# Optimization experiments

Hardware: AMD Instinct MI355X
Metric: run time of the kernel (lower is better)

## Reference

```python
import jax, jax.numpy as jnp
import numpy as np

B, L, D = 2, 2048, 1024
H, G = 16, 2            # num_heads, num_kv_groups
HPG = H // G            # heads per kv group = 8
DQK, DV = 128, 128      # qk_head_dim, v_head_dim (head_dim=64, ratios=2.0)


def setup_inputs() -> dict:
    key = jax.random.key(0)
    ks = jax.random.split(key, 12)

    def xavier(k, shape, scale=1.0):
        fan_in, fan_out = shape[0], shape[1]
        lim = np.sqrt(6.0 / (fan_in + fan_out))
        return jax.random.uniform(k, shape, jnp.float32, -lim, lim) * scale

    return {
        "in_q": jax.random.normal(ks[0], (B, L, D), jnp.float32),
        "in_k": jax.random.normal(ks[1], (B, L, D), jnp.float32),
        "in_v": jax.random.normal(ks[2], (B, L, D), jnp.float32),
        # weights stored as [in, out] (transpose of torch Linear); qk_init_scale=0.5
        "Wq": xavier(ks[3], (D, H * DQK), 0.5),
        "bq": jnp.zeros((H * DQK,), jnp.float32),
        "Wk": xavier(ks[4], (D, G * DQK), 0.5),
        "bk": jnp.zeros((G * DQK,), jnp.float32),
        "Wv": xavier(ks[5], (D, G * DV)),
        "bv": jnp.zeros((G * DV,), jnp.float32),
        "Wo": xavier(ks[6], (H * DV, D)),
        "bo": jnp.zeros((D,), jnp.float32),
        "q_extra_scale": jnp.ones((1,), jnp.float32),
    }


def reference(in_q, in_k, in_v, Wq, bq, Wk, bk, Wv, bv, Wo, bo, q_extra_scale):
    # fused projections
    q = (in_q @ Wq + bq) * q_extra_scale              # [B,L,H*DQK]
    k = in_k @ Wk + bk                                 # [B,L,G*DQK]
    v = in_v @ Wv + bv                                 # [B,L,G*DV]

    # reshape: keep GQA group structure instead of materializing repeat_interleave
    q = q.reshape(B, L, G, HPG, DQK)                   # heads grouped: head h = g*HPG + m
    k = k.reshape(B, L, G, DQK)
    v = v.reshape(B, L, G, DV)

    scale = 1.0 / np.sqrt(DQK)
    # scores: [B,G,HPG,L_q,L_kv]
    scores = jnp.einsum("bsgmd,btgd->bgmst", q, k) * scale
    causal = jnp.tril(jnp.ones((L, L), bool))          # is_causal=True
    scores = jnp.where(causal, scores, jnp.finfo(scores.dtype).min)
    attn = jax.nn.softmax(scores, axis=-1)
    ctx = jnp.einsum("bgmst,btgd->bsgmd", attn, v)     # [B,L,G,HPG,DV]
    ctx = ctx.reshape(B, L, H * DV)
    return ctx @ Wo + bo                               # [B,L,D]
```

## Files before the change

### kernel.cpp

```cpp
#include <hip/hip_runtime.h>


typedef __bf16 bf16;
typedef __bf16 bf16x8 __attribute__((ext_vector_type(8)));
typedef __bf16 bf16x4 __attribute__((ext_vector_type(4)));
typedef float f32x4 __attribute__((ext_vector_type(4)));
typedef float f32x16 __attribute__((ext_vector_type(16)));
typedef float float4v __attribute__((ext_vector_type(4)));

#define MFMA_BF16(a, b, c) __builtin_amdgcn_mfma_f32_16x16x32_bf16((a), (b), (c), 0, 0, 0)
#define MFMA32(a, b, c)    __builtin_amdgcn_mfma_f32_32x32x16_bf16((a), (b), (c), 0, 0, 0)

static constexpr int Bz = 2, Lz = 2048, Dz = 1024;
static constexpr int Hz = 16, Gz = 2;
static constexpr int DQKz = 128, DVz = 128;

__device__ __forceinline__ void async_copy16(const bf16* g, bf16* l) {
    __builtin_amdgcn_global_load_lds(
        (const __attribute__((address_space(1))) unsigned int*)g,
        (__attribute__((address_space(3))) unsigned int*)l, 16, 0, 0);
}

__device__ __forceinline__ unsigned cvt_pk_bf16(float lo, float hi) {
    unsigned r;
    asm("v_cvt_pk_bf16_f32 %0, %1, %2" : "=v"(r) : "v"(lo), "v"(hi));
    return r;
}

__global__ __launch_bounds__(256) void prep(
    const float* __restrict__ q, const float* __restrict__ k,
    const float* __restrict__ v, bf16* __restrict__ dq,
    bf16* __restrict__ dk, bf16* __restrict__ dv,
    const float* __restrict__ Wq, const float* __restrict__ Wk,
    const float* __restrict__ Wv, const float* __restrict__ Wo,
    bf16* __restrict__ WqT, bf16* __restrict__ WkT,
    bf16* __restrict__ WvT, bf16* __restrict__ WoT)
{
    int bid = blockIdx.x;
    if (bid < 6144) {
        const float* s = bid < 2048 ? q : (bid < 4096 ? k : v);
        bf16* d = bid < 2048 ? dq : (bid < 4096 ? dk : dv);
        int i = (bid & 2047) * 2048 + threadIdx.x * 8;
        float4v a = *(const float4v*)(s + i);
        float4v b = *(const float4v*)(s + i + 4);
        bf16x8 o;
        #pragma unroll
        for (int j = 0; j < 4; ++j) { o[j] = (bf16)a[j]; o[j + 4] = (bf16)b[j]; }
        *(bf16x8*)(d + i) = o;
        return;
    }
    bid -= 6144;
    const float* W; bf16* WT; int K, N;
    if (bid < 2048)      { W = Wq; WT = WqT; K = 1024; N = 2048; }
    else if (bid < 2304) { W = Wk; WT = WkT; K = 1024; N = 256;  bid -= 2048; }
    else if (bid < 2560) { W = Wv; WT = WvT; K = 1024; N = 256;  bid -= 2304; }
    else                 { W = Wo; WT = WoT; K = 2048; N = 1024; bid -= 2560; }
    int tiles_n = N >> 5;
    int n0 = (bid % tiles_n) * 32, k0 = (bid / tiles_n) * 32;

    __shared__ bf16 t[32][33];
    int tx = threadIdx.x & 31, ty = threadIdx.x >> 5;
    #pragma unroll
    for (int i = 0; i < 4; ++i)
        t[ty + i * 8][tx] = (bf16)W[(size_t)(k0 + ty + i * 8) * N + n0 + tx];
    __syncthreads();
    #pragma unroll
    for (int i = 0; i < 4; ++i)
        WT[(size_t)(n0 + ty + i * 8) * K + k0 + tx] = t[tx][ty + i * 8];
}

template <typename TC>
__device__ __forceinline__ void gemm_tile(
    const bf16* __restrict__ A, const bf16* __restrict__ BT,
    const float* __restrict__ bias, float scale, TC* __restrict__ C,
    int M, int N, int K, int m0, int n0, bool trans_out,
    bf16 (&As)[2][128 * 64], bf16 (&Bs)[2][128 * 64])
{
    const int tid  = threadIdx.x;
    const int wave = tid >> 6;
    const int lane = tid & 63;
    const int quad = lane >> 4;
    const int l16  = lane & 15;
    const int sw   = l16 & 7;
    const int wm = wave >> 2, wn = wave & 3;

    f32x4 acc[4][2] = {};

    auto stage = [&](int k0, int buf) {
        #pragma unroll
        for (int s = 0; s < 2; ++s) {
            int i = s * 512 + tid;
            int row = i >> 3, c = (i & 7) ^ (row & 7);
            async_copy16(A + (size_t)(m0 + row) * K + k0 + c * 8, &As[buf][i * 8]);
        }
        #pragma unroll
        for (int s = 0; s < 2; ++s) {
            int i = s * 512 + tid;
            int row = i >> 3, c = (i & 7) ^ (row & 7);
            async_copy16(BT + (size_t)(n0 + row) * K + k0 + c * 8, &Bs[buf][i * 8]);
        }
    };

    stage(0, 0);
    int cur = 0;
    for (int k0 = 0; k0 < K; k0 += 64) {
        __syncthreads();
        if (k0 + 64 < K) stage(k0 + 64, cur ^ 1);

        #pragma unroll
        for (int ks = 0; ks < 2; ++ks) {
            bf16x8 af[4], bfv[2];
            #pragma unroll
            for (int mt = 0; mt < 4; ++mt)
                af[mt] = *(const bf16x8*)(&As[cur][((wm * 64 + mt * 16 + l16) * 8
                                                    + ((ks * 4 + quad) ^ sw)) * 8]);
            #pragma unroll
            for (int nt = 0; nt < 2; ++nt)
                bfv[nt] = *(const bf16x8*)(&Bs[cur][((wn * 32 + nt * 16 + l16) * 8
                                                     + ((ks * 4 + quad) ^ sw)) * 8]);
            #pragma unroll
            for (int mt = 0; mt < 4; ++mt)
                #pragma unroll
                for (int nt = 0; nt < 2; ++nt)
                    acc[mt][nt] = MFMA_BF16(af[mt], bfv[nt], acc[mt][nt]);
        }
        cur ^= 1;
    }

    #pragma unroll
    for (int nt = 0; nt < 2; ++nt) {
        int col = n0 + wn * 32 + nt * 16 + l16;
        float bv = bias[col];
        #pragma unroll
        for (int mt = 0; mt < 4; ++mt) {
            int row = m0 + wm * 64 + mt * 16 + quad * 4;
            if (trans_out) {
                struct V4 { TC v[4]; } o;
                #pragma unroll
                for (int r = 0; r < 4; ++r)
                    o.v[r] = (TC)((acc[mt][nt][r] + bv) * scale);
                *(V4*)(&C[(size_t)col * M + row]) = o;
            } else {
                #pragma unroll
                for (int r = 0; r < 4; ++r)
                    C[(size_t)(row + r) * N + col] =
                        (TC)((acc[mt][nt][r] + bv) * scale);
            }
        }
    }
}

__global__ __launch_bounds__(512, 4) void proj_qkv(
    const bf16* __restrict__ aq, const bf16* __restrict__ ak,
    const bf16* __restrict__ av, const bf16* __restrict__ WqT,
    const bf16* __restrict__ WkT, const bf16* __restrict__ WvT,
    const float* __restrict__ bq, const float* __restrict__ bk,
    const float* __restrict__ bv, const float* __restrict__ qsc,
    bf16* __restrict__ Qw, bf16* __restrict__ Kw, bf16* __restrict__ VwT)
{
    __shared__ bf16 As[2][128 * 64];
    __shared__ bf16 Bs[2][128 * 64];
    int bid = blockIdx.x;
    if (bid < 512) {
        float scale = qsc[0] * 0.08838834764831845f * 1.4426950408889634f;
        gemm_tile<bf16>(aq, WqT, bq, scale, Qw, 4096, 2048, 1024,
                        (bid >> 4) * 128, (bid & 15) * 128, false, As, Bs);
    } else if (bid < 576) {
        int b2 = bid - 512;
        gemm_tile<bf16>(ak, WkT, bk, 1.0f, Kw, 4096, 256, 1024,
                        (b2 >> 1) * 128, (b2 & 1) * 128, false, As, Bs);
    } else {
        int b2 = bid - 576;
        gemm_tile<bf16>(av, WvT, bv, 1.0f, VwT, 4096, 256, 1024,
                        (b2 >> 1) * 128, (b2 & 1) * 128, true, As, Bs);
    }
}

__global__ __launch_bounds__(512, 4) void proj_o(
    const bf16* __restrict__ Cw, const bf16* __restrict__ WoT,
    const float* __restrict__ bo, float* __restrict__ out)
{
    __shared__ bf16 As[2][128 * 64];
    __shared__ bf16 Bs[2][128 * 64];
    gemm_tile<float>(Cw, WoT, bo, 1.0f, out, 4096, 1024, 2048,
                     (blockIdx.x >> 3) * 128, (blockIdx.x & 7) * 128,
                     false, As, Bs);
}

__global__ __launch_bounds__(256, 3) void attn_fused(
    const bf16* __restrict__ Q,
    const bf16* __restrict__ Kp,
    const bf16* __restrict__ VT,
    bf16* __restrict__ ctx)
{
    __shared__ bf16 smem[24576];

    const int tid  = threadIdx.x;
    const int wave = tid >> 6;
    const int lane = tid & 63;
    const int hi   = lane >> 5;
    const int l31  = lane & 31;
    const int s7   = l31 & 7;
    const int wq   = wave >> 1;
    const int kvw  = wave & 1;

    const int h = blockIdx.y;
    const int b = blockIdx.z;
    const int g = h >> 3;

    const bf16* kgbase = Kp + (size_t)(b * Lz) * (Gz * DQKz) + g * DQKz;
    const bf16* vgbase = VT + (size_t)(g * DVz) * (Bz * Lz) + b * Lz;

    int kgo[4], vgo[4], ldso[4];
    #pragma unroll
    for (int s = 0; s < 4; ++s) {
        int i = s * 256 + tid;
        ldso[s] = i * 8;
        int key = i >> 4, ck = (i & 15) ^ (key & 7);
        kgo[s] = key * (Gz * DQKz) + ck * 8;
        int dvr = i >> 3, cv = (i & 7) ^ (dvr & 7);
        vgo[s] = dvr * (Bz * Lz) + cv * 8;
    }
    auto stage_K = [&](int kt) {
        const bf16* kb = kgbase + (size_t)(kt * 64) * (Gz * DQKz);
        #pragma unroll
        for (int s = 0; s < 4; ++s) async_copy16(kb + kgo[s], smem + ldso[s]);
    };
    auto stage_V = [&](int kt, int buf) {
        const bf16* vb = vgbase + kt * 64;
        #pragma unroll
        for (int s = 0; s < 4; ++s)
            async_copy16(vb + vgo[s], smem + 8192 + buf * 8192 + ldso[s]);
    };

    int koff[8];
    #pragma unroll
    for (int ks = 0; ks < 8; ++ks)
        koff[ks] = ((kvw * 32 + l31) * 16 + ((ks * 2 + hi) ^ s7)) * 8;
    int voff[4][2];
    #pragma unroll
    for (int dt = 0; dt < 4; ++dt)
        #pragma unroll
        for (int kss = 0; kss < 2; ++kss)
            voff[dt][kss] = ((dt * 32 + l31) * 8
                             + ((kvw * 4 + kss * 2 + hi) ^ s7)) * 8;

    const int qt  = 31 - (int)blockIdx.x;
    const int q0  = qt * 64;
    const int nkt = qt + 1;
    const int qrow = q0 + wq * 32 + l31;

    bf16x8 qf[8];
    {
        const bf16* qbase = Q + (size_t)(b * Lz + qrow) * (Hz * DQKz) + h * DQKz;
        #pragma unroll
        for (int s = 0; s < 8; ++s)
            qf[s] = *(const bf16x8*)(qbase + s * 16 + hi * 8);
    }

    f32x16 oacc0 = {}, oacc1 = {}, oacc2 = {}, oacc3 = {};
    float lsum = 0.0f;

    stage_K(0);
    stage_V(0, 0);
    int cur = 0;

    for (int kt = 0; kt < nkt; ++kt) {
        __syncthreads();

        const bf16* vcur = smem + 8192 + cur * 8192;

        f32x16 sacc = {};
        __builtin_amdgcn_s_setprio(1);
        #pragma unroll
        for (int ks = 0; ks < 8; ++ks) {
            bf16x8 kf = *(const bf16x8*)(smem + koff[ks]);
            sacc = MFMA32(kf, qf[ks], sacc);
        }
        __builtin_amdgcn_s_setprio(0);

        __syncthreads();
        if (kt + 1 < nkt) {
            stage_K(kt + 1);
            stage_V(kt + 1, cur ^ 1);
        }

        float pv[16];
        if (kt == nkt - 1) {
            #pragma unroll
            for (int r = 0; r < 16; ++r) {
                int key = kvw * 32 + (r & 3) + 8 * (r >> 2) + 4 * hi;
                pv[r] = (key > wq * 32 + l31) ? 0.0f
                                              : exp2f(sacc[r] - 8.0f);
            }
        } else {
            #pragma unroll
            for (int r = 0; r < 16; ++r)
                pv[r] = exp2f(sacc[r] - 8.0f);
        }
        lsum += ((pv[0] + pv[1]) + (pv[2] + pv[3]))
              + ((pv[4] + pv[5]) + (pv[6] + pv[7]))
              + ((pv[8] + pv[9]) + (pv[10] + pv[11]))
              + ((pv[12] + pv[13]) + (pv[14] + pv[15]));

        unsigned c0 = cvt_pk_bf16(pv[0],  pv[1]);
        unsigned c1 = cvt_pk_bf16(pv[2],  pv[3]);
        unsigned c2 = cvt_pk_bf16(pv[4],  pv[5]);
        unsigned c3 = cvt_pk_bf16(pv[6],  pv[7]);
        unsigned c4 = cvt_pk_bf16(pv[8],  pv[9]);
        unsigned c5 = cvt_pk_bf16(pv[10], pv[11]);
        unsigned c6 = cvt_pk_bf16(pv[12], pv[13]);
        unsigned c7 = cvt_pk_bf16(pv[14], pv[15]);
        asm("v_permlane32_swap_b32 %0, %1" : "+v"(c0), "+v"(c2));
        asm("v_permlane32_swap_b32 %0, %1" : "+v"(c1), "+v"(c3));
        asm("v_permlane32_swap_b32 %0, %1" : "+v"(c4), "+v"(c6));
        asm("v_permlane32_swap_b32 %0, %1" : "+v"(c5), "+v"(c7));
        union { unsigned u[4]; bf16x8 v; } p0 = {{c0, c1, c2, c3}};
        union { unsigned u[4]; bf16x8 v; } p1 = {{c4, c5, c6, c7}};

        __builtin_amdgcn_s_setprio(1);
        {
            bf16x8 vf;
            vf = *(const bf16x8*)(vcur + voff[0][0]); oacc0 = MFMA32(vf, p0.v, oacc0);
            vf = *(const bf16x8*)(vcur + voff[0][1]); oacc0 = MFMA32(vf, p1.v, oacc0);
            vf = *(const bf16x8*)(vcur + voff[1][0]); oacc1 = MFMA32(vf, p0.v, oacc1);
            vf = *(const bf16x8*)(vcur + voff[1][1]); oacc1 = MFMA32(vf, p1.v, oacc1);
            vf = *(const bf16x8*)(vcur + voff[2][0]); oacc2 = MFMA32(vf, p0.v, oacc2);
            vf = *(const bf16x8*)(vcur + voff[2][1]); oacc2 = MFMA32(vf, p1.v, oacc2);
            vf = *(const bf16x8*)(vcur + voff[3][0]); oacc3 = MFMA32(vf, p0.v, oacc3);
            vf = *(const bf16x8*)(vcur + voff[3][1]); oacc3 = MFMA32(vf, p1.v, oacc3);
        }
        __builtin_amdgcn_s_setprio(0);
        cur ^= 1;
    }

    lsum += __shfl_xor(lsum, 32);

    float* SM = (float*)smem;
    float* E0 = SM;
    float* E1 = SM + 5120;
    float* LS = SM + 10240;
    __syncthreads();

    auto store_partial = [&](f32x16 v, float* E) {
        #pragma unroll
        for (int j = 0; j < 4; ++j) {
            f32x4 v4 = { v[4 * j], v[4 * j + 1], v[4 * j + 2], v[4 * j + 3] };
            *(f32x4*)&E[(wave * 64 + lane) * 20 + 4 * j] = v4;
        }
    };
    if (kvw == 0) { store_partial(oacc2, E0); store_partial(oacc3, E1); }
    else          { store_partial(oacc0, E0); store_partial(oacc1, E1); }
    if (lane < 32) LS[wave * 32 + lane] = lsum;
    __syncthreads();
    lsum += LS[(wave ^ 1) * 32 + l31];
    const float inv = 1.0f / lsum;

    bf16* cbase = ctx + (size_t)(b * Lz + qrow) * (Hz * DVz) + h * DVz;
    auto finalize = [&](f32x16 v, float* E, int dt) {
        #pragma unroll
        for (int j = 0; j < 4; ++j) {
            f32x4 p4 = *(const f32x4*)&E[((wave ^ 1) * 64 + lane) * 20 + 4 * j];
            bf16x4 o4;
            #pragma unroll
            for (int r = 0; r < 4; ++r)
                o4[r] = (bf16)((v[4 * j + r] + p4[r]) * inv);
            *(bf16x4*)&cbase[dt * 32 + j * 8 + hi * 4] = o4;
        }
    };
    if (kvw == 0) { finalize(oacc0, E0, 0); finalize(oacc1, E1, 1); }
    else          { finalize(oacc2, E0, 2); finalize(oacc3, E1, 3); }
}

extern "C" void kernel_launch(void* const* d_in, const int* in_sizes, int n_in,
                              void* d_out, int out_size, void* d_ws, size_t ws_size,
                              hipStream_t stream)
{
    (void)in_sizes; (void)n_in; (void)out_size; (void)ws_size;

    const float* in_q = (const float*)d_in[0];
    const float* in_k = (const float*)d_in[1];
    const float* in_v = (const float*)d_in[2];
    const float* Wq   = (const float*)d_in[3];
    const float* bq   = (const float*)d_in[4];
    const float* Wk   = (const float*)d_in[5];
    const float* bk   = (const float*)d_in[6];
    const float* Wv   = (const float*)d_in[7];
    const float* bv   = (const float*)d_in[8];
    const float* Wo   = (const float*)d_in[9];
    const float* bo   = (const float*)d_in[10];
    const float* qsc  = (const float*)d_in[11];
    float* out = (float*)d_out;

    const int M = Bz * Lz;
    const int NQ = Hz * DQKz;
    const int NKV = Gz * DQKz;

    bf16* aq  = (bf16*)d_ws;
    bf16* WqT = aq  + (size_t)M * Dz;
    bf16* WkT = WqT + (size_t)NQ * Dz;
    bf16* WvT = WkT + (size_t)NKV * Dz;
    bf16* WoT = WvT + (size_t)NKV * Dz;
    bf16* Qw  = WoT + (size_t)Dz * NQ;
    bf16* Kw  = Qw  + (size_t)M * NQ;
    bf16* VwT = Kw  + (size_t)M * NKV;
    bf16* Cw  = VwT + (size_t)NKV * M;
    bf16* ak  = Cw;
    bf16* av  = Cw + (size_t)M * Dz;

    prep<<<dim3(10752), dim3(256), 0, stream>>>(
        in_q, in_k, in_v, aq, ak, av, Wq, Wk, Wv, Wo, WqT, WkT, WvT, WoT);

    proj_qkv<<<dim3(640), dim3(512), 0, stream>>>(
        aq, ak, av, WqT, WkT, WvT, bq, bk, bv, qsc, Qw, Kw, VwT);

    attn_fused<<<dim3(32, Hz, Bz), dim3(256), 0, stream>>>(Qw, Kw, VwT, Cw);

    proj_o<<<dim3(256), dim3(512), 0, stream>>>(Cw, WoT, bo, out);
}
```

Baseline: 281.7 us.

## Pair causal query tiles per block and software-pipeline QK with double-buffered K

```diff
diff --git a/kernel.cpp b/kernel.cpp
--- a/kernel.cpp
+++ b/kernel.cpp
@@ -187,13 +187,13 @@
                      false, As, Bs);
 }
 
-__global__ __launch_bounds__(256, 3) void attn_fused(
+__global__ __launch_bounds__(256, 2) void attn_fused(
     const bf16* __restrict__ Q,
     const bf16* __restrict__ Kp,
     const bf16* __restrict__ VT,
     bf16* __restrict__ ctx)
 {
-    __shared__ bf16 smem[24576];
+    __shared__ bf16 smem[32768];
 
     const int tid  = threadIdx.x;
     const int wave = tid >> 6;
@@ -221,16 +221,17 @@
         int dvr = i >> 3, cv = (i & 7) ^ (dvr & 7);
         vgo[s] = dvr * (Bz * Lz) + cv * 8;
     }
-    auto stage_K = [&](int kt) {
+    auto stage_K = [&](int kt, int buf) {
         const bf16* kb = kgbase + (size_t)(kt * 64) * (Gz * DQKz);
         #pragma unroll
-        for (int s = 0; s < 4; ++s) async_copy16(kb + kgo[s], smem + ldso[s]);
+        for (int s = 0; s < 4; ++s)
+            async_copy16(kb + kgo[s], smem + buf * 8192 + ldso[s]);
     };
     auto stage_V = [&](int kt, int buf) {
         const bf16* vb = vgbase + kt * 64;
         #pragma unroll
         for (int s = 0; s < 4; ++s)
-            async_copy16(vb + vgo[s], smem + 8192 + buf * 8192 + ldso[s]);
+            async_copy16(vb + vgo[s], smem + 16384 + buf * 8192 + ldso[s]);
     };
 
     int koff[8];
@@ -245,131 +246,149 @@
             voff[dt][kss] = ((dt * 32 + l31) * 8
                              + ((kvw * 4 + kss * 2 + hi) ^ s7)) * 8;
 
-    const int qt  = 31 - (int)blockIdx.x;
-    const int q0  = qt * 64;
-    const int nkt = qt + 1;
-    const int qrow = q0 + wq * 32 + l31;
-
-    bf16x8 qf[8];
-    {
-        const bf16* qbase = Q + (size_t)(b * Lz + qrow) * (Hz * DQKz) + h * DQKz;
-        #pragma unroll
-        for (int s = 0; s < 8; ++s)
-            qf[s] = *(const bf16x8*)(qbase + s * 16 + hi * 8);
-    }
-
-    f32x16 oacc0 = {}, oacc1 = {}, oacc2 = {}, oacc3 = {};
-    float lsum = 0.0f;
-
-    stage_K(0);
-    stage_V(0, 0);
-    int cur = 0;
-
-    for (int kt = 0; kt < nkt; ++kt) {
+    for (int pass = 0; pass < 2; ++pass) {
+        const int qt  = pass == 0 ? (31 - (int)blockIdx.x) : (int)blockIdx.x;
+        const int q0  = qt * 64;
+        const int nkt = qt + 1;
+        const int qrow = q0 + wq * 32 + l31;
+
+        bf16x8 qf[8];
+        {
+            const bf16* qbase = Q + (size_t)(b * Lz + qrow) * (Hz * DQKz) + h * DQKz;
+            #pragma unroll
+            for (int s = 0; s < 8; ++s)
+                qf[s] = *(const bf16x8*)(qbase + s * 16 + hi * 8);
+        }
+
+        f32x16 oacc0 = {}, oacc1 = {}, oacc2 = {}, oacc3 = {};
+        f32x16 saccA = {}, saccB = {};
+        float lsum = 0.0f;
+
+        if (pass) __syncthreads();
+        stage_K(0, 0);
+        stage_V(0, 0);
+        if (nkt > 1) stage_K(1, 1);
         __syncthreads();
 
-        const bf16* vcur = smem + 8192 + cur * 8192;
-
-        f32x16 sacc = {};
-        __builtin_amdgcn_s_setprio(1);
-        #pragma unroll
-        for (int ks = 0; ks < 8; ++ks) {
-            bf16x8 kf = *(const bf16x8*)(smem + koff[ks]);
-            sacc = MFMA32(kf, qf[ks], sacc);
-        }
-        __builtin_amdgcn_s_setprio(0);
-
+        {
+            f32x16 s = {};
+            #pragma unroll
+            for (int ks = 0; ks < 8; ++ks) {
+                bf16x8 kf = *(const bf16x8*)(smem + koff[ks]);
+                s = MFMA32(kf, qf[ks], s);
+            }
+            saccA = s;
+        }
+
+        auto iter_body = [&](int t, f32x16& scur, f32x16& snxt) {
+            __syncthreads();
+            if (t + 2 < nkt) stage_K(t + 2, t & 1);
+            if (t + 1 < nkt) stage_V(t + 1, (t + 1) & 1);
+
+            if (t + 1 < nkt) {
+                const bf16* kc = smem + ((t + 1) & 1) * 8192;
+                f32x16 s = {};
+                #pragma unroll
+                for (int ks = 0; ks < 8; ++ks) {
+                    bf16x8 kf = *(const bf16x8*)(kc + koff[ks]);
+                    s = MFMA32(kf, qf[ks], s);
+                }
+                snxt = s;
+            }
+
+            float pv[16];
+            if (t == nkt - 1) {
+                #pragma unroll
+                for (int r = 0; r < 16; ++r) {
+                    int key = kvw * 32 + (r & 3) + 8 * (r >> 2) + 4 * hi;
+                    pv[r] = (key > wq * 32 + l31) ? 0.0f
+                                                  : exp2f(scur[r] - 8.0f);
+                }
+            } else {
+                #pragma unroll
+                for (int r = 0; r < 16; ++r)
+                    pv[r] = exp2f(scur[r] - 8.0f);
+            }
+            lsum += ((pv[0] + pv[1]) + (pv[2] + pv[3]))
+                  + ((pv[4] + pv[5]) + (pv[6] + pv[7]))
+                  + ((pv[8] + pv[9]) + (pv[10] + pv[11]))
+                  + ((pv[12] + pv[13]) + (pv[14] + pv[15]));
+
+            unsigned c0 = cvt_pk_bf16(pv[0],  pv[1]);
+            unsigned c1 = cvt_pk_bf16(pv[2],  pv[3]);
+            unsigned c2 = cvt_pk_bf16(pv[4],  pv[5]);
+            unsigned c3 = cvt_pk_bf16(pv[6],  pv[7]);
+            unsigned c4 = cvt_pk_bf16(pv[8],  pv[9]);
+            unsigned c5 = cvt_pk_bf16(pv[10], pv[11]);
+            unsigned c6 = cvt_pk_bf16(pv[12], pv[13]);
+            unsigned c7 = cvt_pk_bf16(pv[14], pv[15]);
+            asm("v_permlane32_swap_b32 %0, %1" : "+v"(c0), "+v"(c2));
+            asm("v_permlane32_swap_b32 %0, %1" : "+v"(c1), "+v"(c3));
+            asm("v_permlane32_swap_b32 %0, %1" : "+v"(c4), "+v"(c6));
+            asm("v_permlane32_swap_b32 %0, %1" : "+v"(c5), "+v"(c7));
+            union { unsigned u[4]; bf16x8 v; } p0 = {{c0, c1, c2, c3}};
+            union { unsigned u[4]; bf16x8 v; } p1 = {{c4, c5, c6, c7}};
+
+            const bf16* vcur = smem + 16384 + (t & 1) * 8192;
+            __builtin_amdgcn_s_setprio(1);
+            {
+                bf16x8 vf;
+                vf = *(const bf16x8*)(vcur + voff[0][0]); oacc0 = MFMA32(vf, p0.v, oacc0);
+                vf = *(const bf16x8*)(vcur + voff[0][1]); oacc0 = MFMA32(vf, p1.v, oacc0);
+                vf = *(const bf16x8*)(vcur + voff[1][0]); oacc1 = MFMA32(vf, p0.v, oacc1);
+                vf = *(const bf16x8*)(vcur + voff[1][1]); oacc1 = MFMA32(vf, p1.v, oacc1);
+                vf = *(const bf16x8*)(vcur + voff[2][0]); oacc2 = MFMA32(vf, p0.v, oacc2);
+                vf = *(const bf16x8*)(vcur + voff[2][1]); oacc2 = MFMA32(vf, p1.v, oacc2);
+                vf = *(const bf16x8*)(vcur + voff[3][0]); oacc3 = MFMA32(vf, p0.v, oacc3);
+                vf = *(const bf16x8*)(vcur + voff[3][1]); oacc3 = MFMA32(vf, p1.v, oacc3);
+            }
+            __builtin_amdgcn_s_setprio(0);
+        };
+
+        int t = 0;
+        for (; t + 2 <= nkt; t += 2) {
+            iter_body(t,     saccA, saccB);
+            iter_body(t + 1, saccB, saccA);
+        }
+        if (nkt & 1) iter_body(nkt - 1, saccA, saccB);
+
+        lsum += __shfl_xor(lsum, 32);
+
+        float* SM = (float*)smem;
+        float* E0 = SM;
+        float* E1 = SM + 5120;
+        float* LS = SM + 10240;
         __syncthreads();
-        if (kt + 1 < nkt) {
-            stage_K(kt + 1);
-            stage_V(kt + 1, cur ^ 1);
-        }
-
-        float pv[16];
-        if (kt == nkt - 1) {
-            #pragma unroll
-            for (int r = 0; r < 16; ++r) {
-                int key = kvw * 32 + (r & 3) + 8 * (r >> 2) + 4 * hi;
-                pv[r] = (key > wq * 32 + l31) ? 0.0f
-                                              : exp2f(sacc[r] - 8.0f);
-            }
-        } else {
-            #pragma unroll
-            for (int r = 0; r < 16; ++r)
-                pv[r] = exp2f(sacc[r] - 8.0f);
-        }
-        lsum += ((pv[0] + pv[1]) + (pv[2] + pv[3]))
-              + ((pv[4] + pv[5]) + (pv[6] + pv[7]))
-              + ((pv[8] + pv[9]) + (pv[10] + pv[11]))
-              + ((pv[12] + pv[13]) + (pv[14] + pv[15]));
-
-        unsigned c0 = cvt_pk_bf16(pv[0],  pv[1]);
-        unsigned c1 = cvt_pk_bf16(pv[2],  pv[3]);
-        unsigned c2 = cvt_pk_bf16(pv[4],  pv[5]);
-        unsigned c3 = cvt_pk_bf16(pv[6],  pv[7]);
-        unsigned c4 = cvt_pk_bf16(pv[8],  pv[9]);
-        unsigned c5 = cvt_pk_bf16(pv[10], pv[11]);
-        unsigned c6 = cvt_pk_bf16(pv[12], pv[13]);
-        unsigned c7 = cvt_pk_bf16(pv[14], pv[15]);
-        asm("v_permlane32_swap_b32 %0, %1" : "+v"(c0), "+v"(c2));
-        asm("v_permlane32_swap_b32 %0, %1" : "+v"(c1), "+v"(c3));
-        asm("v_permlane32_swap_b32 %0, %1" : "+v"(c4), "+v"(c6));
-        asm("v_permlane32_swap_b32 %0, %1" : "+v"(c5), "+v"(c7));
-        union { unsigned u[4]; bf16x8 v; } p0 = {{c0, c1, c2, c3}};
-        union { unsigned u[4]; bf16x8 v; } p1 = {{c4, c5, c6, c7}};
-
-        __builtin_amdgcn_s_setprio(1);
-        {
-            bf16x8 vf;
-            vf = *(const bf16x8*)(vcur + voff[0][0]); oacc0 = MFMA32(vf, p0.v, oacc0);
-            vf = *(const bf16x8*)(vcur + voff[0][1]); oacc0 = MFMA32(vf, p1.v, oacc0);
-            vf = *(const bf16x8*)(vcur + voff[1][0]); oacc1 = MFMA32(vf, p0.v, oacc1);
-            vf = *(const bf16x8*)(vcur + voff[1][1]); oacc1 = MFMA32(vf, p1.v, oacc1);
-            vf = *(const bf16x8*)(vcur + voff[2][0]); oacc2 = MFMA32(vf, p0.v, oacc2);
-            vf = *(const bf16x8*)(vcur + voff[2][1]); oacc2 = MFMA32(vf, p1.v, oacc2);
-            vf = *(const bf16x8*)(vcur + voff[3][0]); oacc3 = MFMA32(vf, p0.v, oacc3);
-            vf = *(const bf16x8*)(vcur + voff[3][1]); oacc3 = MFMA32(vf, p1.v, oacc3);
-        }
-        __builtin_amdgcn_s_setprio(0);
-        cur ^= 1;
-    }
-
-    lsum += __shfl_xor(lsum, 32);
-
-    float* SM = (float*)smem;
-    float* E0 = SM;
-    float* E1 = SM + 5120;
-    float* LS = SM + 10240;
-    __syncthreads();
-
-    auto store_partial = [&](f32x16 v, float* E) {
-        #pragma unroll
-        for (int j = 0; j < 4; ++j) {
-            f32x4 v4 = { v[4 * j], v[4 * j + 1], v[4 * j + 2], v[4 * j + 3] };
-            *(f32x4*)&E[(wave * 64 + lane) * 20 + 4 * j] = v4;
-        }
-    };
-    if (kvw == 0) { store_partial(oacc2, E0); store_partial(oacc3, E1); }
-    else          { store_partial(oacc0, E0); store_partial(oacc1, E1); }
-    if (lane < 32) LS[wave * 32 + lane] = lsum;
-    __syncthreads();
-    lsum += LS[(wave ^ 1) * 32 + l31];
-    const float inv = 1.0f / lsum;
-
-    bf16* cbase = ctx + (size_t)(b * Lz + qrow) * (Hz * DVz) + h * DVz;
-    auto finalize = [&](f32x16 v, float* E, int dt) {
-        #pragma unroll
-        for (int j = 0; j < 4; ++j) {
-            f32x4 p4 = *(const f32x4*)&E[((wave ^ 1) * 64 + lane) * 20 + 4 * j];
-            bf16x4 o4;
-            #pragma unroll
-            for (int r = 0; r < 4; ++r)
-                o4[r] = (bf16)((v[4 * j + r] + p4[r]) * inv);
-            *(bf16x4*)&cbase[dt * 32 + j * 8 + hi * 4] = o4;
-        }
-    };
-    if (kvw == 0) { finalize(oacc0, E0, 0); finalize(oacc1, E1, 1); }
-    else          { finalize(oacc2, E0, 2); finalize(oacc3, E1, 3); }
+
+        auto store_partial = [&](f32x16 v, float* E) {
+            #pragma unroll
+            for (int j = 0; j < 4; ++j) {
+                f32x4 v4 = { v[4 * j], v[4 * j + 1], v[4 * j + 2], v[4 * j + 3] };
+                *(f32x4*)&E[(wave * 64 + lane) * 20 + 4 * j] = v4;
+            }
+        };
+        if (kvw == 0) { store_partial(oacc2, E0); store_partial(oacc3, E1); }
+        else          { store_partial(oacc0, E0); store_partial(oacc1, E1); }
+        if (lane < 32) LS[wave * 32 + lane] = lsum;
+        __syncthreads();
+        lsum += LS[(wave ^ 1) * 32 + l31];
+        const float inv = 1.0f / lsum;
+
+        bf16* cbase = ctx + (size_t)(b * Lz + qrow) * (Hz * DVz) + h * DVz;
+        auto finalize = [&](f32x16 v, float* E, int dt) {
+            #pragma unroll
+            for (int j = 0; j < 4; ++j) {
+                f32x4 p4 = *(const f32x4*)&E[((wave ^ 1) * 64 + lane) * 20 + 4 * j];
+                bf16x4 o4;
+                #pragma unroll
+                for (int r = 0; r < 4; ++r)
+                    o4[r] = (bf16)((v[4 * j + r] + p4[r]) * inv);
+                *(bf16x4*)&cbase[dt * 32 + j * 8 + hi * 4] = o4;
+            }
+        };
+        if (kvw == 0) { finalize(oacc0, E0, 0); finalize(oacc1, E1, 1); }
+        else          { finalize(oacc2, E0, 2); finalize(oacc3, E1, 3); }
+    }
 }
 
 extern "C" void kernel_launch(void* const* d_in, const int* in_sizes, int n_in,
@@ -414,7 +433,7 @@
     proj_qkv<<<dim3(640), dim3(512), 0, stream>>>(
         aq, ak, av, WqT, WkT, WvT, bq, bk, bv, qsc, Qw, Kw, VwT);
 
-    attn_fused<<<dim3(32, Hz, Bz), dim3(256), 0, stream>>>(Qw, Kw, VwT, Cw);
+    attn_fused<<<dim3(16, Hz, Bz), dim3(256), 0, stream>>>(Qw, Kw, VwT, Cw);
 
     proj_o<<<dim3(256), dim3(512), 0, stream>>>(Cw, WoT, bo, out);
 }
```

Measured after the change: 248.3 us. -11.8%, faster.
